# Kernel optimization log

Measured on AMD Instinct MI355X. Metric: run time of the kernel, lower is better.

## Reference

```python
import jax, jax.numpy as jnp
import numpy as np

B, L = 1024, 64          # sentences, tokens per sentence
V, E = 100000, 300       # vocab, embedding dim
RH, M, NC = 50, 50, 3    # rnn_hidden, mem_dim, num_class
N = B * L                # total tree nodes


def setup_inputs() -> dict:
    key = jax.random.key(0)
    ks = jax.random.split(key, 24)
    rn = lambda k, s, sc=0.05: jax.random.normal(k, s, dtype=jnp.float32) * sc
    # balanced binary dependency tree per sentence: parent(i) = (i-1)//2
    loc = np.arange(L)
    par_loc = np.where(loc == 0, -1, (loc - 1) // 2)
    parent = np.where(par_loc[None, :] < 0, -1,
                      par_loc[None, :] + np.arange(B)[:, None] * L).reshape(-1)
    depth = np.tile(np.floor(np.log2(loc + 1)).astype(np.int64), B)
    tm = np.zeros(L, np.float32); tm[1:4] = 1.0  # 3 aspect-target tokens/sentence
    return {
        "embed_ids": jax.random.randint(ks[0], (B, L), 0, V),
        "parent": jnp.asarray(parent),
        "depth": jnp.asarray(depth),
        "target_mask": jnp.asarray(np.tile(tm, B)),
        "num_levels": 7,
        "embed_table": rn(ks[1], (V, E), 1.0),
        "W_ih_f": rn(ks[2], (4 * RH, E)), "W_hh_f": rn(ks[3], (4 * RH, RH)),
        "b_f": rn(ks[4], (4 * RH,)),
        "W_ih_b": rn(ks[5], (4 * RH, E)), "W_hh_b": rn(ks[6], (4 * RH, RH)),
        "b_b": rn(ks[7], (4 * RH,)),
        "W_iou": rn(ks[8], (3 * M, 2 * RH)),
        "U_iou_w": rn(ks[9], (3 * M, M)), "U_iou_b": rn(ks[10], (3 * M,)),
        "b_iou": jnp.zeros((3 * M,), jnp.float32),
        "U_f_w": rn(ks[11], (M, M)), "U_f_b": rn(ks[12], (M,)),
        "H_w": rn(ks[13], (M, 2 * RH)), "H_b": rn(ks[14], (M,)),
        "C_w": rn(ks[15], (NC, M)), "C_b": rn(ks[16], (NC,)),
    }


def _lstm(x, W_ih, W_hh, b, reverse):
    # x: (B, L, E) -> (B, L, H); PyTorch gate order i, f, g, o
    xg = jnp.einsum('ble,ge->blg', x, W_ih) + b
    H = W_hh.shape[1]
    def step(carry, xt):
        h, c = carry
        g = xt + h @ W_hh.T
        i, f, gg, o = jnp.split(g, 4, axis=-1)
        c = jax.nn.sigmoid(f) * c + jax.nn.sigmoid(i) * jnp.tanh(gg)
        h = jax.nn.sigmoid(o) * jnp.tanh(c)
        return (h, c), h
    z = jnp.zeros((x.shape[0], H), x.dtype)
    _, hs = jax.lax.scan(step, (z, z), jnp.swapaxes(xg, 0, 1), reverse=reverse)
    return jnp.swapaxes(hs, 0, 1)


def reference(embed_ids, parent, depth, target_mask, num_levels, embed_table,
              W_ih_f, W_hh_f, b_f, W_ih_b, W_hh_b, b_b,
              W_iou, U_iou_w, U_iou_b, b_iou, U_f_w, U_f_b,
              H_w, H_b, C_w, C_b):
    # --- BiLSTM encoder (dropout = identity at inference) ---
    emb = embed_table[embed_ids]                       # (B,L,E) gather
    hf = _lstm(emb, W_ih_f, W_hh_f, b_f, False)
    hb = _lstm(emb, W_ih_b, W_hh_b, b_b, True)
    x = jnp.concatenate([hf, hb], -1).reshape(N, 2 * RH)
    # --- ChildSum TreeLSTM, topological (deepest level first) ---
    iou0 = x @ W_iou.T                                 # (N, 3M)
    h_init = x @ H_w.T + H_b                           # (N, M)
    parent_safe = jnp.where(parent >= 0, parent, N)    # roots -> dummy slot N
    counts = jnp.zeros(N + 1, jnp.int32).at[parent_safe].add(1)
    has_children = (counts[:N] > 0)[:, None]
    h_fin = h_init
    c_fin = jnp.zeros((N, M), jnp.float32)
    h_sum = jnp.zeros((N + 1, M), jnp.float32)         # sum of child h
    fc_sum = jnp.zeros((N + 1, M), jnp.float32)        # sum of f * child c
    for lvl in range(num_levels - 1, -1, -1):
        m = (depth == lvl)[:, None]
        # reduce: leaves never get U_iou bias (no mailbox in DGL)
        iou = iou0 + jnp.where(has_children, h_sum[:N] @ U_iou_w.T + U_iou_b, 0.0) + b_iou
        i, o, u = jnp.split(iou, 3, axis=-1)
        c_new = jax.nn.sigmoid(i) * jnp.tanh(u) + fc_sum[:N]
        h_new = h_init + jax.nn.sigmoid(o) * jnp.tanh(c_new)
        h_fin = jnp.where(m, h_new, h_fin)
        c_fin = jnp.where(m, c_new, c_fin)
        # scatter messages from this level's nodes to their parents
        f = jax.nn.sigmoid(h_new @ U_f_w.T + U_f_b)
        h_sum = h_sum.at[parent_safe].add(jnp.where(m, h_new, 0.0))
        fc_sum = fc_sum.at[parent_safe].add(jnp.where(m, f * c_new, 0.0))
    # --- masked mean pool over target tokens per sentence ---
    tm = target_mask.reshape(B, L)
    pooled = (h_fin.reshape(B, L, M) * tm[:, :, None]).sum(1) / tm.sum(1, keepdims=True)
    logits = pooled @ C_w.T + C_b
    return logits, pooled
```

## Files before the change

kernel.cpp:

```cpp
#include <hip/hip_runtime.h>


typedef __attribute__((ext_vector_type(8))) short bf16x8;
typedef __attribute__((ext_vector_type(4))) float f32x4;

__device__ __forceinline__ float fsig(float x) { return 1.0f / (1.0f + __expf(-x)); }
__device__ __forceinline__ float ftanh(float x) {
    float a = fabsf(x);
    float t = __expf(2.0f * a);
    float r = 1.0f - 2.0f / (t + 1.0f);
    return copysignf(r, x);
}
__device__ __forceinline__ float fsig2(float x) {
    float e = __builtin_amdgcn_exp2f(-1.4426950408889634f * x);
    return __builtin_amdgcn_rcpf(1.0f + e);
}
__device__ __forceinline__ float ftanh2(float x) {
    float e = __builtin_amdgcn_exp2f(2.8853900817779268f * x);
    return 1.0f - 2.0f * __builtin_amdgcn_rcpf(1.0f + e);
}

__device__ __forceinline__ unsigned short rne_bf16(float f) {
    unsigned u = __builtin_bit_cast(unsigned, f);
    unsigned r = u + 0x7fffu + ((u >> 16) & 1u);
    return (unsigned short)(r >> 16);
}
__device__ __forceinline__ void split2(float f, unsigned short& h, unsigned short& l) {
    h = rne_bf16(f);
    float fh = __builtin_bit_cast(float, ((unsigned)h) << 16);
    float r = f - fh;
    l = rne_bf16(r);
}

__device__ __forceinline__ void async_lds16(const void* g, void* l) {
    __builtin_amdgcn_global_load_lds(
        (const __attribute__((address_space(1))) unsigned int*)g,
        (__attribute__((address_space(3))) unsigned int*)l, 16, 0, 0);
}

__device__ __forceinline__ bf16x8 pack8(const unsigned short* h) {
    bf16x8 v;
    #pragma unroll
    for (int e = 0; e < 8; ++e) v[e] = (short)h[e];
    return v;
}

__device__ __forceinline__ void conv_item(int q, const float* __restrict__ B1,
                                          const float* __restrict__ B2,
                                          int split, int K, int Rreal, int BN,
                                          unsigned short* __restrict__ out) {
    int n  = q % BN;
    int kq = (q / BN) & 3;
    int c  = q / (BN * 4);
    const float* row = (n < split) ? (B1 + (size_t)n * K) : (B2 + (size_t)(n - split) * K);
    unsigned short h[8], l[8];
    #pragma unroll
    for (int e = 0; e < 8; ++e) {
        int k = c * 32 + kq * 8 + e;
        float v = (n < Rreal && k < K) ? row[k] : 0.0f;
        split2(v, h[e], l[e]);
    }
    size_t hb = ((((size_t)c * 2 + 0) * 4 + kq) * BN + n) * 8;
    size_t lb = ((((size_t)c * 2 + 1) * 4 + kq) * BN + n) * 8;
    *(ushort4*)&out[hb]     = make_ushort4(h[0], h[1], h[2], h[3]);
    *(ushort4*)&out[hb + 4] = make_ushort4(h[4], h[5], h[6], h[7]);
    *(ushort4*)&out[lb]     = make_ushort4(l[0], l[1], l[2], l[3]);
    *(ushort4*)&out[lb + 4] = make_ushort4(l[4], l[5], l[6], l[7]);
}

constexpr int WHC_DIR = 2 * 2 * 4 * 208 * 8;

__global__ void conv_fused(const float* __restrict__ Wihf, const float* __restrict__ Wihb,
                           const float* __restrict__ Wiou, const float* __restrict__ Hw,
                           const float* __restrict__ Whhf, const float* __restrict__ Whhb,
                           unsigned short* __restrict__ B1c,
                           unsigned short* __restrict__ B3c,
                           unsigned short* __restrict__ Whc) {
    int q = blockIdx.x * 256 + threadIdx.x;
    if (q < 17920) {
        conv_item(q, Wihf, Wihb, 200, 300, 400, 448, B1c);
    } else if (q < 22016) {
        conv_item(q - 17920, Wiou, Hw, 150, 100, 200, 256, B3c);
    } else if (q < 23680) {
        conv_item(q - 22016, Whhf, Whhf, 200, 50, 200, 208, Whc);
    } else if (q < 25344) {
        conv_item(q - 23680, Whhb, Whhb, 200, 50, 200, 208, Whc + WHC_DIR);
    }
}

template<int BN, int KCH, int KREAL, int NCOLS, bool GATHER>
__global__ __launch_bounds__(256)
void gemm_split(const float* __restrict__ A, const int* __restrict__ ids,
                const unsigned short* __restrict__ Bc,
                const float* __restrict__ bias1, const float* __restrict__ bias2,
                int split, float* __restrict__ C) {
    constexpr int NTW = BN / 64;
    __shared__ __align__(16) unsigned short As[2 * 4 * 64 * 8];
    __shared__ __align__(16) unsigned short Bt[64 * BN];

    const int tid = threadIdx.x;
    const int m0 = blockIdx.x * 64;
    const int w = tid >> 6, lane = tid & 63;
    const int r16 = lane & 15, quad = lane >> 4;
    const int wn = w * (BN / 4);

    const int mA = tid & 63, kqA = tid >> 6;
    const float* arow = GATHER ? (A + (size_t)ids[m0 + mA] * KREAL)
                               : (A + (size_t)(m0 + mA) * KREAL);

    float ar[8];
    {
        int k0 = kqA * 8;
        if (k0 + 8 <= KREAL) {
            float4 p = *(const float4*)(arow + k0);
            float4 q = *(const float4*)(arow + k0 + 4);
            ar[0]=p.x; ar[1]=p.y; ar[2]=p.z; ar[3]=p.w;
            ar[4]=q.x; ar[5]=q.y; ar[6]=q.z; ar[7]=q.w;
        } else {
            #pragma unroll
            for (int e = 0; e < 8; ++e) ar[e] = (k0 + e < KREAL) ? arow[k0 + e] : 0.0f;
        }
    }

    f32x4 acc[4][NTW] = {};

    for (int c = 0; c < KCH; ++c) {
        __syncthreads();
        {
            const unsigned short* src = Bc + (size_t)c * 64 * BN + tid * 8;
            #pragma unroll
            for (int i = 0; i < BN / 32; ++i)
                async_lds16(src + (size_t)i * 2048, Bt + i * 2048 + tid * 8);
        }
        {
            unsigned short h[8], l[8];
            #pragma unroll
            for (int e = 0; e < 8; ++e) split2(ar[e], h[e], l[e]);
            *(bf16x8*)&As[((0 * 4 + kqA) * 64 + mA) * 8] = pack8(h);
            *(bf16x8*)&As[((1 * 4 + kqA) * 64 + mA) * 8] = pack8(l);
        }
        __syncthreads();
        if (c + 1 < KCH) {
            int k0 = (c + 1) * 32 + kqA * 8;
            if (k0 + 8 <= KREAL) {
                float4 p = *(const float4*)(arow + k0);
                float4 q = *(const float4*)(arow + k0 + 4);
                ar[0]=p.x; ar[1]=p.y; ar[2]=p.z; ar[3]=p.w;
                ar[4]=q.x; ar[5]=q.y; ar[6]=q.z; ar[7]=q.w;
            } else {
                #pragma unroll
                for (int e = 0; e < 8; ++e) ar[e] = (k0 + e < KREAL) ? arow[k0 + e] : 0.0f;
            }
        }
        bf16x8 af[2][4];
        #pragma unroll
        for (int i = 0; i < 4; ++i) {
            af[0][i] = *(const bf16x8*)&As[((0 * 4 + quad) * 64 + i * 16 + r16) * 8];
            af[1][i] = *(const bf16x8*)&As[((1 * 4 + quad) * 64 + i * 16 + r16) * 8];
        }
        #pragma unroll
        for (int t = 0; t < NTW; ++t) {
            bf16x8 bh = *(const bf16x8*)&Bt[((0 * 4 + quad) * BN + wn + t * 16 + r16) * 8];
            bf16x8 bl = *(const bf16x8*)&Bt[((1 * 4 + quad) * BN + wn + t * 16 + r16) * 8];
            #pragma unroll
            for (int i = 0; i < 4; ++i) {
                acc[i][t] = __builtin_amdgcn_mfma_f32_16x16x32_bf16(af[0][i], bh, acc[i][t], 0, 0, 0);
                acc[i][t] = __builtin_amdgcn_mfma_f32_16x16x32_bf16(af[1][i], bh, acc[i][t], 0, 0, 0);
                acc[i][t] = __builtin_amdgcn_mfma_f32_16x16x32_bf16(af[0][i], bl, acc[i][t], 0, 0, 0);
            }
        }
    }

    #pragma unroll
    for (int t = 0; t < NTW; ++t) {
        int ncol = wn + t * 16 + r16;
        if (ncol < NCOLS) {
            float bv = (ncol < split) ? bias1[ncol] : bias2[ncol - split];
            #pragma unroll
            for (int i = 0; i < 4; ++i)
                #pragma unroll
                for (int r = 0; r < 4; ++r) {
                    int mrow = m0 + i * 16 + quad * 4 + r;
                    C[(size_t)mrow * NCOLS + ncol] = acc[i][t][r] + bv;
                }
        }
    }
}

__global__ __launch_bounds__(256)
void lstm_mfma(const float* __restrict__ xg, const unsigned short* __restrict__ Whc,
               float* __restrict__ x) {
    const int bi = blockIdx.x;
    const int dir = bi & 1;
    const int b0 = (bi >> 1) * 8;
    const int tid = threadIdx.x;
    const int w = tid >> 6, lane = tid & 63;
    const int r16 = lane & 15, quad = lane >> 4;

    __shared__ __align__(16) unsigned short Ah[8 * 16 * 8];
    __shared__ __align__(16) unsigned short Al[8 * 16 * 8];
    __shared__ __align__(16) float G[208 * 20];
    __shared__ __align__(16) float Xs[3][8][268];

    const int n0 = (w == 0) ? 0 : (w == 1) ? 4 : (w == 2) ? 7 : 10;
    const int nc = (w == 0) ? 4 : 3;

    const unsigned short* Wd = Whc + (size_t)dir * WHC_DIR;
    bf16x8 bfr[4][2][2];
    #pragma unroll
    for (int t = 0; t < 4; ++t) {
        int col = (n0 + ((t < nc) ? t : 0)) * 16 + r16;
        #pragma unroll
        for (int c = 0; c < 2; ++c)
            #pragma unroll
            for (int h = 0; h < 2; ++h)
                bfr[t][c][h] = *(const bf16x8*)&Wd[((((size_t)c * 2 + h) * 4 + quad) * 208 + col) * 8];
    }

    for (int q = tid; q < 512; q += 256) {
        ((unsigned*)Ah)[q] = 0u;
        ((unsigned*)Al)[q] = 0u;
    }

    int ss[2], ms[2];
    bool act[2];
    #pragma unroll
    for (int j = 0; j < 2; ++j) {
        int q = w * 100 + lane + 64 * j;
        ss[j] = q & 7;
        ms[j] = q >> 3;
        act[j] = (lane + 64 * j) < 100;
    }
    float c_reg[2] = {0.0f, 0.0f};

    #pragma unroll
    for (int p = 0; p < 2; ++p) {
        int idx0 = dir ? (63 - p) : p;
        #pragma unroll
        for (int i = 0; i < 2; ++i) {
            int s = w * 2 + i;
            const float* src = xg + ((size_t)(b0 + s) * 64 + idx0) * 400 + dir * 200 + lane * 4;
            async_lds16(src, &Xs[p][s][lane * 4]);
        }
    }
    __syncthreads();

    for (int step = 0; step < 64; ++step) {
        const int buf = step % 3;
        const int idx = dir ? (63 - step) : step;
        {
            int stepn = step + 2; if (stepn > 63) stepn = 63;
            const int slot = (step + 2) % 3;
            const int idxn = dir ? (63 - stepn) : stepn;
            #pragma unroll
            for (int i = 0; i < 2; ++i) {
                int s = w * 2 + i;
                const float* src = xg + ((size_t)(b0 + s) * 64 + idxn) * 400 + dir * 200 + lane * 4;
                async_lds16(src, &Xs[slot][s][lane * 4]);
            }
            __builtin_amdgcn_sched_barrier(0);
        }
        bf16x8 ah[2], al[2];
        #pragma unroll
        for (int c = 0; c < 2; ++c) {
            ah[c] = *(const bf16x8*)&Ah[((c * 4 + quad) * 16 + r16) * 8];
            al[c] = *(const bf16x8*)&Al[((c * 4 + quad) * 16 + r16) * 8];
        }
        f32x4 acc[4] = {};
        #pragma unroll
        for (int t = 0; t < 4; ++t) {
            if (t < nc) {
                #pragma unroll
                for (int c = 0; c < 2; ++c) {
                    acc[t] = __builtin_amdgcn_mfma_f32_16x16x32_bf16(ah[c], bfr[t][c][0], acc[t], 0, 0, 0);
                    acc[t] = __builtin_amdgcn_mfma_f32_16x16x32_bf16(al[c], bfr[t][c][0], acc[t], 0, 0, 0);
                    acc[t] = __builtin_amdgcn_mfma_f32_16x16x32_bf16(ah[c], bfr[t][c][1], acc[t], 0, 0, 0);
                }
            }
        }
        #pragma unroll
        for (int t = 0; t < 4; ++t) {
            if (t < nc) {
                int col = (n0 + t) * 16 + r16;
                *(f32x4*)&G[col * 20 + quad * 4] = acc[t];
            }
        }
        asm volatile("s_waitcnt lgkmcnt(0) vmcnt(8)" ::: "memory");
        __builtin_amdgcn_sched_barrier(0);
        __builtin_amdgcn_s_barrier();
        __builtin_amdgcn_sched_barrier(0);
        #pragma unroll
        for (int j = 0; j < 2; ++j) {
            if (act[j]) {
                int s = ss[j], m = ms[j];
                float gi = G[m * 20 + s]         + Xs[buf][s][m];
                float gf = G[(m + 50) * 20 + s]  + Xs[buf][s][m + 50];
                float gg = G[(m + 100) * 20 + s] + Xs[buf][s][m + 100];
                float go = G[(m + 150) * 20 + s] + Xs[buf][s][m + 150];
                c_reg[j] = fsig2(gf) * c_reg[j] + fsig2(gi) * ftanh2(gg);
                float h = fsig2(go) * ftanh2(c_reg[j]);
                unsigned short hh, hl;
                split2(h, hh, hl);
                Ah[(m >> 3) * 128 + s * 8 + (m & 7)] = hh;
                Al[(m >> 3) * 128 + s * 8 + (m & 7)] = hl;
                x[((size_t)(b0 + s) * 64 + idx) * 100 + dir * 50 + m] = h;
            }
        }
        asm volatile("s_waitcnt lgkmcnt(0)" ::: "memory");
        __builtin_amdgcn_sched_barrier(0);
        __builtin_amdgcn_s_barrier();
        __builtin_amdgcn_sched_barrier(0);
    }
}

__global__ __launch_bounds__(256)
void tree_kernel(const float* __restrict__ C2,
                 const float* __restrict__ Uw, const float* __restrict__ Ub,
                 const float* __restrict__ Fw, const float* __restrict__ Fb,
                 const float* __restrict__ tmask,
                 const float* __restrict__ Cw, const float* __restrict__ Cb,
                 float* __restrict__ out) {
    const int b = blockIdx.x;
    const int tid = threadIdx.x;

    __shared__ __align__(16) float h_sum[32][52];
    __shared__ __align__(16) float fc_sum[32][52];
    __shared__ __align__(16) float hcur[32][52];
    __shared__ __align__(16) float mcur[32][52];
    __shared__ float msg[16][152];
    __shared__ float hfin[64][50];
    __shared__ float pool[52];

    const int rU = (tid < 150) ? tid : 0;
    const int rF = tid % 50;
    float ur[50], fr[50];
    #pragma unroll
    for (int k = 0; k < 50; ++k) ur[k] = Uw[rU * 50 + k];
    #pragma unroll
    for (int k = 0; k < 50; ++k) fr[k] = Fw[rF * 50 + k];
    const float ub = Ub[rU];
    const float fb = Fb[rF];

    for (int q = tid; q < 32 * 52; q += 256) {
        h_sum[q / 52][q % 52] = 0.0f;
        fc_sum[q / 52][q % 52] = 0.0f;
    }
    __syncthreads();

    const float* c2b = C2 + (size_t)b * 64 * 200;

    for (int lvl = 6; lvl >= 0; --lvl) {
        const int lo = (1 << lvl) - 1;
        const int hi = min((1 << (lvl + 1)) - 2, 63);
        const int A = hi - lo + 1;
        const int chn = max(0, min(hi, 31) - lo + 1);

        if (tid < 150) {
            for (int a = 0; a < chn; ++a) {
                float acc = ub;
                #pragma unroll
                for (int k4 = 0; k4 < 12; ++k4) {
                    float4 h4 = *(const float4*)&h_sum[lo + a][k4 * 4];
                    acc += ur[k4*4+0]*h4.x + ur[k4*4+1]*h4.y + ur[k4*4+2]*h4.z + ur[k4*4+3]*h4.w;
                }
                acc += ur[48]*h_sum[lo + a][48] + ur[49]*h_sum[lo + a][49];
                msg[a][tid] = acc;
            }
        }
        __syncthreads();

        for (int q = tid; q < A * 50; q += 256) {
            int a = q / 50, m = q - a * 50;
            int loc = lo + a;
            const float* base = c2b + (size_t)loc * 200;
            bool ch = (a < chn);
            float ig = base[m]       + (ch ? msg[a][m]       : 0.0f);
            float og = base[50 + m]  + (ch ? msg[a][50 + m]  : 0.0f);
            float ug = base[100 + m] + (ch ? msg[a][100 + m] : 0.0f);
            float cn = fsig(ig) * ftanh(ug) + (ch ? fc_sum[loc][m] : 0.0f);
            float hn = base[150 + m] + fsig(og) * ftanh(cn);
            hcur[a][m] = hn;
            mcur[a][m] = cn;
            hfin[loc][m] = hn;
        }
        __syncthreads();

        if (tid < 250) {
            for (int a = tid / 50; a < A; a += 5) {
                float acc = fb;
                #pragma unroll
                for (int k4 = 0; k4 < 12; ++k4) {
                    float4 h4 = *(const float4*)&hcur[a][k4 * 4];
                    acc += fr[k4*4+0]*h4.x + fr[k4*4+1]*h4.y + fr[k4*4+2]*h4.z + fr[k4*4+3]*h4.w;
                }
                acc += fr[48]*hcur[a][48] + fr[49]*hcur[a][49];
                mcur[a][rF] = fsig(acc) * mcur[a][rF];
            }
        }
        __syncthreads();

        if (lvl > 0) {
            const int plo = (lo - 1) >> 1, phi = (hi - 1) >> 1;
            const int P = phi - plo + 1;
            for (int q = tid; q < P * 50; q += 256) {
                int pi = q / 50, m = q - pi * 50;
                int p = plo + pi;
                int c1 = 2 * p + 1, c2i = 2 * p + 2;
                float hs = hcur[c1 - lo][m];
                float fs = mcur[c1 - lo][m];
                if (c2i <= hi) { hs += hcur[c2i - lo][m]; fs += mcur[c2i - lo][m]; }
                h_sum[p][m] += hs;
                fc_sum[p][m] += fs;
            }
        }
        __syncthreads();
    }

    const float* tm = tmask + (size_t)b * 64;
    if (tid < 50) {
        float acc = 0.0f, ws = 0.0f;
        for (int l = 0; l < 64; ++l) {
            float wv = tm[l];
            ws += wv;
            acc += wv * hfin[l][tid];
        }
        float p = acc / ws;
        pool[tid] = p;
        out[3072 + (size_t)b * 50 + tid] = p;
    }
    __syncthreads();
    if (tid < 3) {
        float acc = Cb[tid];
        #pragma unroll
        for (int m = 0; m < 50; ++m) acc += Cw[tid * 50 + m] * pool[m];
        out[(size_t)b * 3 + tid] = acc;
    }
}

extern "C" void kernel_launch(void* const* d_in, const int* in_sizes, int n_in,
                              void* d_out, int out_size, void* d_ws, size_t ws_size,
                              hipStream_t stream) {
    (void)in_sizes; (void)n_in; (void)out_size; (void)ws_size;
    const int*   ids   = (const int*)d_in[0];
    const float* tmask = (const float*)d_in[3];
    const float* table = (const float*)d_in[5];
    const float* Wihf  = (const float*)d_in[6];
    const float* Whhf  = (const float*)d_in[7];
    const float* bf    = (const float*)d_in[8];
    const float* Wihb  = (const float*)d_in[9];
    const float* Whhb  = (const float*)d_in[10];
    const float* bb    = (const float*)d_in[11];
    const float* Wiou  = (const float*)d_in[12];
    const float* Uiouw = (const float*)d_in[13];
    const float* Uioub = (const float*)d_in[14];
    const float* biou  = (const float*)d_in[15];
    const float* Ufw   = (const float*)d_in[16];
    const float* Ufb   = (const float*)d_in[17];
    const float* Hw    = (const float*)d_in[18];
    const float* Hb    = (const float*)d_in[19];
    const float* Cw    = (const float*)d_in[20];
    const float* Cb    = (const float*)d_in[21];
    float* out = (float*)d_out;

    float* wsf = (float*)d_ws;
    float* xg = wsf;
    float* x  = wsf + (size_t)65536 * 400;
    float* C2 = wsf;
    unsigned short* B1c = (unsigned short*)(wsf + 32768000);
    unsigned short* B3c = (unsigned short*)(wsf + 32911360);
    unsigned short* Whc = (unsigned short*)(wsf + 32944128);

    conv_fused<<<99, 256, 0, stream>>>(Wihf, Wihb, Wiou, Hw, Whhf, Whhb,
                                       B1c, B3c, Whc);
    gemm_split<448, 10, 300, 400, true><<<1024, 256, 0, stream>>>(
        table, ids, B1c, bf, bb, 200, xg);
    lstm_mfma<<<256, 256, 0, stream>>>(xg, Whc, x);
    gemm_split<256, 4, 100, 200, false><<<1024, 256, 0, stream>>>(
        x, nullptr, B3c, biou, Hb, 150, C2);
    tree_kernel<<<1024, 256, 0, stream>>>(
        C2, Uiouw, Uioub, Ufw, Ufb, tmask, Cw, Cb, out);
}
```

Before: 423.6 us.

## Redistribute tree-LSTM matvecs across all threads and read weights from global

The U_iou and U_f matvecs in the tree kernel previously kept weight rows in per-thread registers (100 floats each) with a fixed thread-to-row mapping. They now use a flat (node, column) work distribution over all 256 threads and stream weight rows from global/L1 with float4 loads and split accumulators. The aim is lower register pressure and better thread utilisation at narrow levels, at the cost of re-reading the weights every level. It also swaps the activations for exp2/rcp intrinsic versions, caches the target mask in shared memory, and splits the pooling reduction across 200 threads.

After: 462.6 us. +9.2%, slower.

```diff
diff --git a/kernel.cpp b/kernel.cpp
--- a/kernel.cpp
+++ b/kernel.cpp
@@ -4,13 +4,6 @@
 typedef __attribute__((ext_vector_type(8))) short bf16x8;
 typedef __attribute__((ext_vector_type(4))) float f32x4;
 
-__device__ __forceinline__ float fsig(float x) { return 1.0f / (1.0f + __expf(-x)); }
-__device__ __forceinline__ float ftanh(float x) {
-    float a = fabsf(x);
-    float t = __expf(2.0f * a);
-    float r = 1.0f - 2.0f / (t + 1.0f);
-    return copysignf(r, x);
-}
 __device__ __forceinline__ float fsig2(float x) {
     float e = __builtin_amdgcn_exp2f(-1.4426950408889634f * x);
     return __builtin_amdgcn_rcpf(1.0f + e);
@@ -330,21 +323,14 @@
     __shared__ float msg[16][152];
     __shared__ float hfin[64][50];
     __shared__ float pool[52];
-
-    const int rU = (tid < 150) ? tid : 0;
-    const int rF = tid % 50;
-    float ur[50], fr[50];
-    #pragma unroll
-    for (int k = 0; k < 50; ++k) ur[k] = Uw[rU * 50 + k];
-    #pragma unroll
-    for (int k = 0; k < 50; ++k) fr[k] = Fw[rF * 50 + k];
-    const float ub = Ub[rU];
-    const float fb = Fb[rF];
+    __shared__ float tms[64];
+    __shared__ float red[4][52];
 
     for (int q = tid; q < 32 * 52; q += 256) {
         h_sum[q / 52][q % 52] = 0.0f;
         fc_sum[q / 52][q % 52] = 0.0f;
     }
+    if (tid < 64) tms[tid] = tmask[(size_t)b * 64 + tid];
     __syncthreads();
 
     const float* c2b = C2 + (size_t)b * 64 * 200;
@@ -355,17 +341,20 @@
         const int A = hi - lo + 1;
         const int chn = max(0, min(hi, 31) - lo + 1);
 
-        if (tid < 150) {
-            for (int a = 0; a < chn; ++a) {
-                float acc = ub;
-                #pragma unroll
-                for (int k4 = 0; k4 < 12; ++k4) {
-                    float4 h4 = *(const float4*)&h_sum[lo + a][k4 * 4];
-                    acc += ur[k4*4+0]*h4.x + ur[k4*4+1]*h4.y + ur[k4*4+2]*h4.z + ur[k4*4+3]*h4.w;
-                }
-                acc += ur[48]*h_sum[lo + a][48] + ur[49]*h_sum[lo + a][49];
-                msg[a][tid] = acc;
-            }
+        for (int q = tid; q < chn * 150; q += 256) {
+            int a = q / 150, col = q - a * 150;
+            const float* urow = Uw + col * 50;
+            const float* hs = &h_sum[lo + a][0];
+            float a0 = 0.0f, a1 = 0.0f, a2 = 0.0f, a3 = 0.0f;
+            #pragma unroll
+            for (int k4 = 0; k4 < 12; ++k4) {
+                float4 u4 = *(const float4*)&urow[k4 * 4];
+                float4 h4 = *(const float4*)&hs[k4 * 4];
+                a0 += u4.x * h4.x; a1 += u4.y * h4.y;
+                a2 += u4.z * h4.z; a3 += u4.w * h4.w;
+            }
+            msg[a][col] = Ub[col] + (a0 + a1) + (a2 + a3)
+                        + urow[48] * hs[48] + urow[49] * hs[49];
         }
         __syncthreads();
 
@@ -377,25 +366,29 @@
             float ig = base[m]       + (ch ? msg[a][m]       : 0.0f);
             float og = base[50 + m]  + (ch ? msg[a][50 + m]  : 0.0f);
             float ug = base[100 + m] + (ch ? msg[a][100 + m] : 0.0f);
-            float cn = fsig(ig) * ftanh(ug) + (ch ? fc_sum[loc][m] : 0.0f);
-            float hn = base[150 + m] + fsig(og) * ftanh(cn);
+            float cn = fsig2(ig) * ftanh2(ug) + (ch ? fc_sum[loc][m] : 0.0f);
+            float hn = base[150 + m] + fsig2(og) * ftanh2(cn);
             hcur[a][m] = hn;
             mcur[a][m] = cn;
             hfin[loc][m] = hn;
         }
         __syncthreads();
 
-        if (tid < 250) {
-            for (int a = tid / 50; a < A; a += 5) {
-                float acc = fb;
-                #pragma unroll
-                for (int k4 = 0; k4 < 12; ++k4) {
-                    float4 h4 = *(const float4*)&hcur[a][k4 * 4];
-                    acc += fr[k4*4+0]*h4.x + fr[k4*4+1]*h4.y + fr[k4*4+2]*h4.z + fr[k4*4+3]*h4.w;
-                }
-                acc += fr[48]*hcur[a][48] + fr[49]*hcur[a][49];
-                mcur[a][rF] = fsig(acc) * mcur[a][rF];
-            }
+        for (int q = tid; q < A * 50; q += 256) {
+            int a = q / 50, m = q - a * 50;
+            const float* frow = Fw + m * 50;
+            const float* hc = &hcur[a][0];
+            float a0 = 0.0f, a1 = 0.0f, a2 = 0.0f, a3 = 0.0f;
+            #pragma unroll
+            for (int k4 = 0; k4 < 12; ++k4) {
+                float4 f4 = *(const float4*)&frow[k4 * 4];
+                float4 h4 = *(const float4*)&hc[k4 * 4];
+                a0 += f4.x * h4.x; a1 += f4.y * h4.y;
+                a2 += f4.z * h4.z; a3 += f4.w * h4.w;
+            }
+            float acc = Fb[m] + (a0 + a1) + (a2 + a3)
+                      + frow[48] * hc[48] + frow[49] * hc[49];
+            mcur[a][m] = fsig2(acc) * mcur[a][m];
         }
         __syncthreads();
 
@@ -416,14 +409,18 @@
         __syncthreads();
     }
 
-    const float* tm = tmask + (size_t)b * 64;
+    if (tid < 200) {
+        int g = tid / 50, m = tid - g * 50;
+        float part = 0.0f;
+        for (int l = g; l < 64; l += 4) part += tms[l] * hfin[l][m];
+        red[g][m] = part;
+    }
+    __syncthreads();
     if (tid < 50) {
-        float acc = 0.0f, ws = 0.0f;
-        for (int l = 0; l < 64; ++l) {
-            float wv = tm[l];
-            ws += wv;
-            acc += wv * hfin[l][tid];
-        }
+        float ws = 0.0f;
+        #pragma unroll
+        for (int l = 0; l < 64; ++l) ws += tms[l];
+        float acc = red[0][tid] + red[1][tid] + red[2][tid] + red[3][tid];
         float p = acc / ws;
         pool[tid] = p;
         out[3072 + (size_t)b * 50 + tid] = p;
```
